# Performance work log

Measured on AMD Instinct MI355X. Metric: run time of the kernel, lower is better.

## Reference

```python
import jax, jax.numpy as jnp
import numpy as np

N_NODES = 50000


def gcn_conv(h, src, dst, W, b, n):
    # PyG GCNConv: x' = D^{-1/2} (A + I) D^{-1/2} (h W) + b
    x = h @ W  # [N, out]
    deg = jax.ops.segment_sum(jnp.ones_like(src, dtype=x.dtype), dst, num_segments=n) + 1.0  # self-loop
    dis = deg ** -0.5
    norm = dis[src] * dis[dst]  # [E]
    msg = x[src] * norm[:, None]  # [E, out]
    agg = jax.ops.segment_sum(msg, dst, num_segments=n)
    agg = agg + x * (dis * dis)[:, None]  # self-loop term: 1/deg_i * x_i
    return agg + b


def setup_inputs() -> dict:
    key = jax.random.key(0)
    ks = jax.random.split(key, 8)
    n, e = N_NODES, 800000
    d_in, d_rni, h = 128, 32, 256
    x = jax.random.normal(ks[0], (n, d_in), dtype=jnp.float32)
    rni = jax.random.normal(ks[1], (n, d_rni), dtype=jnp.float32)
    edge_index = jax.random.randint(ks[2], (2, e), 0, n, dtype=jnp.int64)
    s1 = (d_in + d_rni) ** -0.5
    s2 = h ** -0.5
    W1 = jax.random.normal(ks[3], (d_in + d_rni, h), dtype=jnp.float32) * s1
    b1 = jnp.zeros((h,), dtype=jnp.float32)
    W2 = jax.random.normal(ks[4], (h, h), dtype=jnp.float32) * s2
    b2 = jnp.zeros((h,), dtype=jnp.float32)
    W_out = jax.random.normal(ks[5], (h, h), dtype=jnp.float32) * s2
    b_out = jnp.zeros((h,), dtype=jnp.float32)
    return {"x": x, "rni": rni, "edge_index": edge_index, "W1": W1, "b1": b1,
            "W2": W2, "b2": b2, "W_out": W_out, "b_out": b_out}


def reference(x, rni, edge_index, W1, b1, W2, b2, W_out, b_out):
    n = x.shape[0]
    src, dst = edge_index[0], edge_index[1]
    h = jnp.concatenate([x, rni], axis=-1)  # RNI concat
    h = jax.nn.relu(gcn_conv(h, src, dst, W1, b1, n))
    h = jax.nn.relu(gcn_conv(h, src, dst, W2, b2, n))
    return h @ W_out + b_out
```

## Files before the change

### kernel.cpp

```cpp
#include <hip/hip_runtime.h>
#include <hip/hip_bf16.h>
#include <hip/hip_fp16.h>
#include <math.h>

#define D_IN   128
#define D_RNI  32
#define HID    256

typedef _Float16 half8 __attribute__((ext_vector_type(8)));
typedef float    f32x4 __attribute__((ext_vector_type(4)));

__global__ void k_detect(const unsigned int* __restrict__ w, int nwords, int* __restrict__ mode) {
    __shared__ unsigned int red[256];
    unsigned int acc = 0;
    for (int i = threadIdx.x; i < 1024; i += 256) {
        int idx = 2 * i + 1;
        if (idx < nwords) acc |= w[idx];
    }
    red[threadIdx.x] = acc;
    __syncthreads();
    for (int s = 128; s > 0; s >>= 1) {
        if (threadIdx.x < s) red[threadIdx.x] |= red[threadIdx.x + s];
        __syncthreads();
    }
    if (threadIdx.x == 0) *mode = (red[0] == 0u) ? 1 : 0;
}

__global__ void k_count(const unsigned int* __restrict__ ew, const int* __restrict__ mode_p,
                        int* __restrict__ counts, int e) {
    int mode = *mode_p;
    int i = blockIdx.x * 256 + threadIdx.x;
    if (i >= e) return;
    int d = mode ? (int)ew[2 * ((size_t)e + i)] : (int)ew[(size_t)e + i];
    atomicAdd(&counts[d], 1);
}

__global__ __launch_bounds__(1024) void k_scan1(const int* __restrict__ counts,
                                                int* __restrict__ incl,
                                                int* __restrict__ bsum, int n) {
    __shared__ int sd[1024];
    int t = threadIdx.x;
    int i = blockIdx.x * 1024 + t;
    int v = (i < n) ? counts[i] : 0;
    sd[t] = v;
    __syncthreads();
    for (int off = 1; off < 1024; off <<= 1) {
        int tmp = (t >= off) ? sd[t - off] : 0;
        __syncthreads();
        sd[t] += tmp;
        __syncthreads();
    }
    if (i < n) incl[i] = sd[t];
    if (t == 1023) bsum[blockIdx.x] = sd[1023];
}

__global__ __launch_bounds__(1024) void k_scan2(int* __restrict__ bsum, int nb) {
    __shared__ int sd[1024];
    int t = threadIdx.x;
    int v = (t < nb) ? bsum[t] : 0;
    sd[t] = v;
    __syncthreads();
    for (int off = 1; off < 1024; off <<= 1) {
        int tmp = (t >= off) ? sd[t - off] : 0;
        __syncthreads();
        sd[t] += tmp;
        __syncthreads();
    }
    if (t < nb) bsum[t] = sd[t] - v;
    if (t == nb - 1) bsum[nb] = sd[t];
}

__global__ void k_scan3(const int* __restrict__ counts, const int* __restrict__ incl,
                        const int* __restrict__ bsum,
                        int* __restrict__ rowptr, int* __restrict__ cursor,
                        float* __restrict__ dis, int n, int nb) {
    int i = blockIdx.x * 256 + threadIdx.x;
    if (i >= n) return;
    int excl = incl[i] - counts[i] + bsum[i >> 10];
    rowptr[i] = excl;
    cursor[i] = excl;
    dis[i] = 1.0f / sqrtf((float)(counts[i] + 1));
    if (i == 0) rowptr[n] = bsum[nb];
}

__global__ void k_scatter(const unsigned int* __restrict__ ew, const int* __restrict__ mode_p,
                          int* __restrict__ cursor, int* __restrict__ csr, int e) {
    int mode = *mode_p;
    int i = blockIdx.x * 256 + threadIdx.x;
    if (i >= e) return;
    int s, d;
    if (mode) {
        s = (int)ew[2 * (size_t)i];
        d = (int)ew[2 * ((size_t)e + i)];
    } else {
        s = (int)ew[(size_t)i];
        d = (int)ew[(size_t)e + i];
    }
    int pos = atomicAdd(&cursor[d], 1);
    csr[pos] = s;
}

__global__ void k_cvt_wt(const float* __restrict__ W, __half* __restrict__ Wt,
                         int K, int N, int total) {
    int i = blockIdx.x * 256 + threadIdx.x;
    if (i >= total) return;
    int k = i / N, nn = i - k * N;
    Wt[(size_t)nn * K + k] = __float2half(W[i]);
}

#define KT 32
#define LSTR 40
template <bool A_F32, bool ADD_BIAS, bool HALF_OUT>
__global__ __launch_bounds__(256) void k_mgemm(const void* __restrict__ Av, int strideA, int KA,
                                               const void* __restrict__ A2v, int strideA2,
                                               const __half* __restrict__ Bt,
                                               const float* __restrict__ bias,
                                               void* Cv, int M, int K) {
    __shared__ __half As[64 * LSTR];
    __shared__ __half Bs[256 * LSTR];
    int tid = threadIdx.x;
    int wave = tid >> 6, lane = tid & 63;
    int q = lane >> 4, m16 = lane & 15;
    int r0 = blockIdx.x * 64;

    f32x4 acc[4][4] = {};

    for (int k0 = 0; k0 < K; k0 += KT) {
        __syncthreads();
        {
            int r = tid >> 2, kq = (tid & 3) * 8;
            int row = r0 + r; if (row >= M) row = M - 1;
            if (A_F32) {
                const float* src; int stride, kk0;
                if (k0 < KA) { src = (const float*)Av;  stride = strideA;  kk0 = k0; }
                else         { src = (const float*)A2v; stride = strideA2; kk0 = k0 - KA; }
                const float* p = &src[(size_t)row * stride + kk0 + kq];
                float4 va = *reinterpret_cast<const float4*>(p);
                float4 vb = *reinterpret_cast<const float4*>(p + 4);
                union { __half2 h2[4]; uint4 u; } uu;
                uu.h2[0] = __floats2half2_rn(va.x, va.y);
                uu.h2[1] = __floats2half2_rn(va.z, va.w);
                uu.h2[2] = __floats2half2_rn(vb.x, vb.y);
                uu.h2[3] = __floats2half2_rn(vb.z, vb.w);
                *reinterpret_cast<uint4*>(&As[r * LSTR + kq]) = uu.u;
            } else {
                const __half* src = (const __half*)Av;
                uint4 v = *reinterpret_cast<const uint4*>(&src[(size_t)row * strideA + k0 + kq]);
                *reinterpret_cast<uint4*>(&As[r * LSTR + kq]) = v;
            }
        }
        {
            int nb = tid >> 2, kq = (tid & 3) * 8;
            #pragma unroll
            for (int i = 0; i < 4; ++i) {
                int nn = nb + i * 64;
                uint4 v = *reinterpret_cast<const uint4*>(&Bt[(size_t)nn * K + k0 + kq]);
                *reinterpret_cast<uint4*>(&Bs[nn * LSTR + kq]) = v;
            }
        }
        __syncthreads();

        half8 af[4], bf[4];
        #pragma unroll
        for (int mi = 0; mi < 4; ++mi)
            af[mi] = *reinterpret_cast<const half8*>(&As[(mi * 16 + m16) * LSTR + q * 8]);
        #pragma unroll
        for (int ni = 0; ni < 4; ++ni)
            bf[ni] = *reinterpret_cast<const half8*>(&Bs[(wave * 64 + ni * 16 + m16) * LSTR + q * 8]);
        #pragma unroll
        for (int mi = 0; mi < 4; ++mi)
            #pragma unroll
            for (int ni = 0; ni < 4; ++ni)
                acc[mi][ni] = __builtin_amdgcn_mfma_f32_16x16x32_f16(af[mi], bf[ni], acc[mi][ni], 0, 0, 0);
    }

    #pragma unroll
    for (int mi = 0; mi < 4; ++mi) {
        #pragma unroll
        for (int r = 0; r < 4; ++r) {
            int row = r0 + mi * 16 + q * 4 + r;
            if (row >= M) continue;
            #pragma unroll
            for (int ni = 0; ni < 4; ++ni) {
                int col = wave * 64 + ni * 16 + m16;
                float v = acc[mi][ni][r];
                if (ADD_BIAS) v += bias[col];
                if (HALF_OUT) ((__half*)Cv)[(size_t)row * HID + col] = __float2half(v);
                else          ((float*)Cv)[(size_t)row * HID + col] = v;
            }
        }
    }
}

__global__ __launch_bounds__(256) void k_agg(const __half* __restrict__ xh,
                                             const int* __restrict__ rowptr,
                                             const int* __restrict__ csr,
                                             const float* __restrict__ dis,
                                             const float* __restrict__ bias,
                                             __half* __restrict__ outh, int n) {
    int i = blockIdx.x * 4 + (threadIdx.x >> 6);
    if (i >= n) return;
    int lane = threadIdx.x & 63;
    int c4 = lane * 4;
    float disd = dis[i];
    int e0 = rowptr[i], e1 = rowptr[i + 1];

    float acc0, acc1, acc2, acc3;
    {
        uint2 v = *reinterpret_cast<const uint2*>(&xh[(size_t)i * HID + c4]);
        float2 f0 = __half22float2(*reinterpret_cast<__half2*>(&v.x));
        float2 f1 = __half22float2(*reinterpret_cast<__half2*>(&v.y));
        float ws = disd * disd;
        acc0 = f0.x * ws; acc1 = f0.y * ws; acc2 = f1.x * ws; acc3 = f1.y * ws;
    }

    for (int e = e0; e < e1; e += 64) {
        int cnt = min(64, e1 - e);
        int sreg = 0; float wreg = 0.0f;
        if (lane < cnt) {
            sreg = csr[e + lane];
            wreg = dis[sreg] * disd;
        }
        int j = 0;
        for (; j + 4 <= cnt; j += 4) {
            int   s0 = __shfl(sreg, j + 0), s1 = __shfl(sreg, j + 1);
            int   s2 = __shfl(sreg, j + 2), s3 = __shfl(sreg, j + 3);
            float w0 = __shfl(wreg, j + 0), w1 = __shfl(wreg, j + 1);
            float w2 = __shfl(wreg, j + 2), w3 = __shfl(wreg, j + 3);
            uint2 v0 = *reinterpret_cast<const uint2*>(&xh[(size_t)s0 * HID + c4]);
            uint2 v1 = *reinterpret_cast<const uint2*>(&xh[(size_t)s1 * HID + c4]);
            uint2 v2 = *reinterpret_cast<const uint2*>(&xh[(size_t)s2 * HID + c4]);
            uint2 v3 = *reinterpret_cast<const uint2*>(&xh[(size_t)s3 * HID + c4]);
            float2 a0 = __half22float2(*reinterpret_cast<__half2*>(&v0.x));
            float2 b0 = __half22float2(*reinterpret_cast<__half2*>(&v0.y));
            float2 a1 = __half22float2(*reinterpret_cast<__half2*>(&v1.x));
            float2 b1 = __half22float2(*reinterpret_cast<__half2*>(&v1.y));
            float2 a2 = __half22float2(*reinterpret_cast<__half2*>(&v2.x));
            float2 b2 = __half22float2(*reinterpret_cast<__half2*>(&v2.y));
            float2 a3 = __half22float2(*reinterpret_cast<__half2*>(&v3.x));
            float2 b3 = __half22float2(*reinterpret_cast<__half2*>(&v3.y));
            acc0 = fmaf(a0.x, w0, acc0); acc1 = fmaf(a0.y, w0, acc1);
            acc2 = fmaf(b0.x, w0, acc2); acc3 = fmaf(b0.y, w0, acc3);
            acc0 = fmaf(a1.x, w1, acc0); acc1 = fmaf(a1.y, w1, acc1);
            acc2 = fmaf(b1.x, w1, acc2); acc3 = fmaf(b1.y, w1, acc3);
            acc0 = fmaf(a2.x, w2, acc0); acc1 = fmaf(a2.y, w2, acc1);
            acc2 = fmaf(b2.x, w2, acc2); acc3 = fmaf(b2.y, w2, acc3);
            acc0 = fmaf(a3.x, w3, acc0); acc1 = fmaf(a3.y, w3, acc1);
            acc2 = fmaf(b3.x, w3, acc2); acc3 = fmaf(b3.y, w3, acc3);
        }
        for (; j < cnt; ++j) {
            int   s = __shfl(sreg, j);
            float w = __shfl(wreg, j);
            uint2 v = *reinterpret_cast<const uint2*>(&xh[(size_t)s * HID + c4]);
            float2 a = __half22float2(*reinterpret_cast<__half2*>(&v.x));
            float2 b = __half22float2(*reinterpret_cast<__half2*>(&v.y));
            acc0 = fmaf(a.x, w, acc0); acc1 = fmaf(a.y, w, acc1);
            acc2 = fmaf(b.x, w, acc2); acc3 = fmaf(b.y, w, acc3);
        }
    }

    float4 bb = *reinterpret_cast<const float4*>(&bias[c4]);
    union { __half2 h2[2]; uint2 u; } o;
    o.h2[0] = __floats2half2_rn(fmaxf(acc0 + bb.x, 0.0f), fmaxf(acc1 + bb.y, 0.0f));
    o.h2[1] = __floats2half2_rn(fmaxf(acc2 + bb.z, 0.0f), fmaxf(acc3 + bb.w, 0.0f));
    *reinterpret_cast<uint2*>(&outh[(size_t)i * HID + c4]) = o.u;
}

extern "C" void kernel_launch(void* const* d_in, const int* in_sizes, int n_in,
                              void* d_out, int out_size, void* d_ws, size_t ws_size,
                              hipStream_t stream) {
    const float* x     = (const float*)d_in[0];
    const float* rni   = (const float*)d_in[1];
    const unsigned int* ew = (const unsigned int*)d_in[2];
    const float* W1    = (const float*)d_in[3];
    const float* b1    = (const float*)d_in[4];
    const float* W2    = (const float*)d_in[5];
    const float* b2    = (const float*)d_in[6];
    const float* W_out = (const float*)d_in[7];
    const float* b_out = (const float*)d_in[8];
    float* out = (float*)d_out;

    const int n  = in_sizes[0] / D_IN;
    const int e  = in_sizes[2] / 2;
    const int nb = (n + 1023) / 1024;
    const int K1 = D_IN + D_RNI;

    char* ws = (char*)d_ws;
    size_t off = 0;
    auto carve = [&](size_t bytes) {
        char* p = ws + off;
        off = (off + bytes + 255) & ~(size_t)255;
        return p;
    };
    __half* xh    = (__half*)carve((size_t)n * HID * sizeof(__half));
    __half* h     = (__half*)carve((size_t)n * HID * sizeof(__half));
    __half* W1t   = (__half*)carve((size_t)K1 * HID * sizeof(__half));
    __half* W2t   = (__half*)carve((size_t)HID * HID * sizeof(__half));
    __half* Wot   = (__half*)carve((size_t)HID * HID * sizeof(__half));
    int*   counts = (int*)carve((size_t)n * sizeof(int));
    int*   incl   = (int*)carve((size_t)n * sizeof(int));
    int*   bsum   = (int*)carve((size_t)(nb + 1) * sizeof(int));
    int*   rowptr = (int*)carve((size_t)(n + 1) * sizeof(int));
    int*   cursor = (int*)carve((size_t)n * sizeof(int));
    float* dis    = (float*)carve((size_t)n * sizeof(float));
    int*   csr    = (int*)carve((size_t)e * sizeof(int));
    int*   mode   = (int*)carve(sizeof(int));
    (void)ws_size;

    const int eb = (e + 255) / 256;
    const int gemm_blocks = (n + 63) / 64;
    const int agg_blocks  = (n + 3) / 4;

    k_detect<<<1, 256, 0, stream>>>(ew, 2 * e, mode);
    hipMemsetAsync(counts, 0, (size_t)n * sizeof(int), stream);
    k_count<<<eb, 256, 0, stream>>>(ew, mode, counts, e);
    k_scan1<<<nb, 1024, 0, stream>>>(counts, incl, bsum, n);
    k_scan2<<<1, 1024, 0, stream>>>(bsum, nb);
    k_scan3<<<(n + 255) / 256, 256, 0, stream>>>(counts, incl, bsum, rowptr, cursor, dis, n, nb);
    k_scatter<<<eb, 256, 0, stream>>>(ew, mode, cursor, csr, e);

    {
        int tw1 = K1 * HID;
        k_cvt_wt<<<(tw1 + 255) / 256, 256, 0, stream>>>(W1, W1t, K1, HID, tw1);
        int tw = HID * HID;
        k_cvt_wt<<<(tw + 255) / 256, 256, 0, stream>>>(W2, W2t, HID, HID, tw);
        k_cvt_wt<<<(tw + 255) / 256, 256, 0, stream>>>(W_out, Wot, HID, HID, tw);
    }

    k_mgemm<true, false, true><<<gemm_blocks, 256, 0, stream>>>(x, D_IN, D_IN, rni, D_RNI,
                                                                W1t, nullptr, xh, n, K1);
    k_agg<<<agg_blocks, 256, 0, stream>>>(xh, rowptr, csr, dis, b1, h, n);

    k_mgemm<false, false, true><<<gemm_blocks, 256, 0, stream>>>(h, HID, HID, nullptr, 0,
                                                                 W2t, nullptr, xh, n, HID);
    k_agg<<<agg_blocks, 256, 0, stream>>>(xh, rowptr, csr, dis, b2, h, n);

    k_mgemm<false, true, false><<<gemm_blocks, 256, 0, stream>>>(h, HID, HID, nullptr, 0,
                                                                 Wot, b_out, out, n, HID);
}
```

Before: 386.1 us.

## Split aggregation columns across 8 blocks and process 8 edges per wave step

The aggregation kernel now launches 8 blocks per group of 4 nodes, each covering a 32-column slice of the 256-wide feature row. Within a wave, 8 lanes handle different edges at once while 8 lanes cover the slice, and the partial sums are combined with xor shuffles. This raises parallelism and memory-level concurrency for low-degree nodes, at the cost of reading csr/dis 8 times per node, extra shuffle reductions, and idle lanes when the edge count is not a multiple of 8. The csr load is also marked nontemporal.

Measured after the change: 607.3 us. +57.3%, slower.

```diff
diff --git a/kernel.cpp b/kernel.cpp
--- a/kernel.cpp
+++ b/kernel.cpp
@@ -198,72 +198,59 @@
                                              const float* __restrict__ dis,
                                              const float* __restrict__ bias,
                                              __half* __restrict__ outh, int n) {
-    int i = blockIdx.x * 4 + (threadIdx.x >> 6);
+    int g = blockIdx.x & 7;
+    int i = (blockIdx.x >> 3) * 4 + (threadIdx.x >> 6);
     if (i >= n) return;
     int lane = threadIdx.x & 63;
-    int c4 = lane * 4;
+    int esub = lane >> 3;
+    int cq   = lane & 7;
+    int cbase = g * 32 + cq * 4;
+    const __half* xcol = xh + cbase;
+
     float disd = dis[i];
     int e0 = rowptr[i], e1 = rowptr[i + 1];
 
-    float acc0, acc1, acc2, acc3;
-    {
-        uint2 v = *reinterpret_cast<const uint2*>(&xh[(size_t)i * HID + c4]);
-        float2 f0 = __half22float2(*reinterpret_cast<__half2*>(&v.x));
-        float2 f1 = __half22float2(*reinterpret_cast<__half2*>(&v.y));
-        float ws = disd * disd;
-        acc0 = f0.x * ws; acc1 = f0.y * ws; acc2 = f1.x * ws; acc3 = f1.y * ws;
-    }
+    float a0 = 0.0f, a1 = 0.0f, a2 = 0.0f, a3 = 0.0f;
 
     for (int e = e0; e < e1; e += 64) {
         int cnt = min(64, e1 - e);
         int sreg = 0; float wreg = 0.0f;
         if (lane < cnt) {
-            sreg = csr[e + lane];
+            sreg = __builtin_nontemporal_load(&csr[e + lane]);
             wreg = dis[sreg] * disd;
         }
-        int j = 0;
-        for (; j + 4 <= cnt; j += 4) {
-            int   s0 = __shfl(sreg, j + 0), s1 = __shfl(sreg, j + 1);
-            int   s2 = __shfl(sreg, j + 2), s3 = __shfl(sreg, j + 3);
-            float w0 = __shfl(wreg, j + 0), w1 = __shfl(wreg, j + 1);
-            float w2 = __shfl(wreg, j + 2), w3 = __shfl(wreg, j + 3);
-            uint2 v0 = *reinterpret_cast<const uint2*>(&xh[(size_t)s0 * HID + c4]);
-            uint2 v1 = *reinterpret_cast<const uint2*>(&xh[(size_t)s1 * HID + c4]);
-            uint2 v2 = *reinterpret_cast<const uint2*>(&xh[(size_t)s2 * HID + c4]);
-            uint2 v3 = *reinterpret_cast<const uint2*>(&xh[(size_t)s3 * HID + c4]);
-            float2 a0 = __half22float2(*reinterpret_cast<__half2*>(&v0.x));
-            float2 b0 = __half22float2(*reinterpret_cast<__half2*>(&v0.y));
-            float2 a1 = __half22float2(*reinterpret_cast<__half2*>(&v1.x));
-            float2 b1 = __half22float2(*reinterpret_cast<__half2*>(&v1.y));
-            float2 a2 = __half22float2(*reinterpret_cast<__half2*>(&v2.x));
-            float2 b2 = __half22float2(*reinterpret_cast<__half2*>(&v2.y));
-            float2 a3 = __half22float2(*reinterpret_cast<__half2*>(&v3.x));
-            float2 b3 = __half22float2(*reinterpret_cast<__half2*>(&v3.y));
-            acc0 = fmaf(a0.x, w0, acc0); acc1 = fmaf(a0.y, w0, acc1);
-            acc2 = fmaf(b0.x, w0, acc2); acc3 = fmaf(b0.y, w0, acc3);
-            acc0 = fmaf(a1.x, w1, acc0); acc1 = fmaf(a1.y, w1, acc1);
-            acc2 = fmaf(b1.x, w1, acc2); acc3 = fmaf(b1.y, w1, acc3);
-            acc0 = fmaf(a2.x, w2, acc0); acc1 = fmaf(a2.y, w2, acc1);
-            acc2 = fmaf(b2.x, w2, acc2); acc3 = fmaf(b2.y, w2, acc3);
-            acc0 = fmaf(a3.x, w3, acc0); acc1 = fmaf(a3.y, w3, acc1);
-            acc2 = fmaf(b3.x, w3, acc2); acc3 = fmaf(b3.y, w3, acc3);
-        }
-        for (; j < cnt; ++j) {
-            int   s = __shfl(sreg, j);
-            float w = __shfl(wreg, j);
-            uint2 v = *reinterpret_cast<const uint2*>(&xh[(size_t)s * HID + c4]);
-            float2 a = __half22float2(*reinterpret_cast<__half2*>(&v.x));
-            float2 b = __half22float2(*reinterpret_cast<__half2*>(&v.y));
-            acc0 = fmaf(a.x, w, acc0); acc1 = fmaf(a.y, w, acc1);
-            acc2 = fmaf(b.x, w, acc2); acc3 = fmaf(b.y, w, acc3);
-        }
-    }
-
-    float4 bb = *reinterpret_cast<const float4*>(&bias[c4]);
-    union { __half2 h2[2]; uint2 u; } o;
-    o.h2[0] = __floats2half2_rn(fmaxf(acc0 + bb.x, 0.0f), fmaxf(acc1 + bb.y, 0.0f));
-    o.h2[1] = __floats2half2_rn(fmaxf(acc2 + bb.z, 0.0f), fmaxf(acc3 + bb.w, 0.0f));
-    *reinterpret_cast<uint2*>(&outh[(size_t)i * HID + c4]) = o.u;
+        for (int j = 0; j < cnt; j += 8) {
+            int   s = __shfl(sreg, j + esub);
+            float w = __shfl(wreg, j + esub);
+            uint2 v = *reinterpret_cast<const uint2*>(&xcol[(size_t)s * HID]);
+            float2 f0 = __half22float2(*reinterpret_cast<__half2*>(&v.x));
+            float2 f1 = __half22float2(*reinterpret_cast<__half2*>(&v.y));
+            a0 = fmaf(f0.x, w, a0); a1 = fmaf(f0.y, w, a1);
+            a2 = fmaf(f1.x, w, a2); a3 = fmaf(f1.y, w, a3);
+        }
+    }
+
+    #pragma unroll
+    for (int m = 8; m < 64; m <<= 1) {
+        a0 += __shfl_xor(a0, m);
+        a1 += __shfl_xor(a1, m);
+        a2 += __shfl_xor(a2, m);
+        a3 += __shfl_xor(a3, m);
+    }
+
+    if (esub == 0) {
+        uint2 v = *reinterpret_cast<const uint2*>(&xcol[(size_t)i * HID]);
+        float2 f0 = __half22float2(*reinterpret_cast<__half2*>(&v.x));
+        float2 f1 = __half22float2(*reinterpret_cast<__half2*>(&v.y));
+        float ws = disd * disd;
+        a0 = fmaf(f0.x, ws, a0); a1 = fmaf(f0.y, ws, a1);
+        a2 = fmaf(f1.x, ws, a2); a3 = fmaf(f1.y, ws, a3);
+        float4 bb = *reinterpret_cast<const float4*>(&bias[cbase]);
+        union { __half2 h2[2]; uint2 u; } o;
+        o.h2[0] = __floats2half2_rn(fmaxf(a0 + bb.x, 0.0f), fmaxf(a1 + bb.y, 0.0f));
+        o.h2[1] = __floats2half2_rn(fmaxf(a2 + bb.z, 0.0f), fmaxf(a3 + bb.w, 0.0f));
+        *reinterpret_cast<uint2*>(&outh[(size_t)i * HID + cbase]) = o.u;
+    }
 }
 
 extern "C" void kernel_launch(void* const* d_in, const int* in_sizes, int n_in,
@@ -309,7 +296,7 @@
 
     const int eb = (e + 255) / 256;
     const int gemm_blocks = (n + 63) / 64;
-    const int agg_blocks  = (n + 3) / 4;
+    const int agg_blocks  = ((n + 3) / 4) * 8;
 
     k_detect<<<1, 256, 0, stream>>>(ew, 2 * e, mode);
     hipMemsetAsync(counts, 0, (size_t)n * sizeof(int), stream);
```

## Enlarge GEMM tile to 128 rows and prefetch next K-slice into registers

Applied to the files above, without the earlier changes.

The dense GEMM kernel now uses 512 threads arranged as a 2x4 wave grid over a 128x256 output tile, which halves how often the shared B-weight tile is reloaded per output row. It also prefetches the next K slice of A and B into registers while the current slice's MFMAs run, so global latency can overlap with compute. In exchange the kernel uses more registers and LDS per block and launches half as many blocks, which may lower occupancy.

After: 368.3 us. 4.6% less time.

```diff
diff --git a/kernel.cpp b/kernel.cpp
--- a/kernel.cpp
+++ b/kernel.cpp
@@ -111,62 +111,77 @@
 #define KT 32
 #define LSTR 40
 template <bool A_F32, bool ADD_BIAS, bool HALF_OUT>
-__global__ __launch_bounds__(256) void k_mgemm(const void* __restrict__ Av, int strideA, int KA,
+__global__ __launch_bounds__(512) void k_mgemm(const void* __restrict__ Av, int strideA, int KA,
                                                const void* __restrict__ A2v, int strideA2,
                                                const __half* __restrict__ Bt,
                                                const float* __restrict__ bias,
                                                void* Cv, int M, int K) {
-    __shared__ __half As[64 * LSTR];
+    __shared__ __half As[128 * LSTR];
     __shared__ __half Bs[256 * LSTR];
     int tid = threadIdx.x;
     int wave = tid >> 6, lane = tid & 63;
+    int wm = wave >> 2, wn = wave & 3;
     int q = lane >> 4, m16 = lane & 15;
-    int r0 = blockIdx.x * 64;
+    int r0 = blockIdx.x * 128;
+
+    int ar  = tid >> 2, akq = (tid & 3) * 8;
+    int br  = tid >> 1, bkq = (tid & 1) * 16;
+
+    int arow = r0 + ar; if (arow >= M) arow = M - 1;
 
     f32x4 acc[4][4] = {};
 
+    float4 afr0, afr1;
+    uint4  areg;
+    uint4  breg0, breg1;
+
+    auto loadA = [&](int k0) {
+        if (A_F32) {
+            const float* src; int stride, kk0;
+            if (k0 < KA) { src = (const float*)Av;  stride = strideA;  kk0 = k0; }
+            else         { src = (const float*)A2v; stride = strideA2; kk0 = k0 - KA; }
+            const float* p = &src[(size_t)arow * stride + kk0 + akq];
+            afr0 = *reinterpret_cast<const float4*>(p);
+            afr1 = *reinterpret_cast<const float4*>(p + 4);
+        } else {
+            const __half* src = (const __half*)Av;
+            areg = *reinterpret_cast<const uint4*>(&src[(size_t)arow * strideA + k0 + akq]);
+        }
+    };
+    auto loadB = [&](int k0) {
+        const __half* p = &Bt[(size_t)br * K + k0 + bkq];
+        breg0 = *reinterpret_cast<const uint4*>(p);
+        breg1 = *reinterpret_cast<const uint4*>(p + 8);
+    };
+    auto writeLDS = [&]() {
+        if (A_F32) {
+            union { __half2 h2[4]; uint4 u; } uu;
+            uu.h2[0] = __floats2half2_rn(afr0.x, afr0.y);
+            uu.h2[1] = __floats2half2_rn(afr0.z, afr0.w);
+            uu.h2[2] = __floats2half2_rn(afr1.x, afr1.y);
+            uu.h2[3] = __floats2half2_rn(afr1.z, afr1.w);
+            *reinterpret_cast<uint4*>(&As[ar * LSTR + akq]) = uu.u;
+        } else {
+            *reinterpret_cast<uint4*>(&As[ar * LSTR + akq]) = areg;
+        }
+        *reinterpret_cast<uint4*>(&Bs[br * LSTR + bkq])     = breg0;
+        *reinterpret_cast<uint4*>(&Bs[br * LSTR + bkq + 8]) = breg1;
+    };
+
+    loadA(0); loadB(0);
     for (int k0 = 0; k0 < K; k0 += KT) {
         __syncthreads();
-        {
-            int r = tid >> 2, kq = (tid & 3) * 8;
-            int row = r0 + r; if (row >= M) row = M - 1;
-            if (A_F32) {
-                const float* src; int stride, kk0;
-                if (k0 < KA) { src = (const float*)Av;  stride = strideA;  kk0 = k0; }
-                else         { src = (const float*)A2v; stride = strideA2; kk0 = k0 - KA; }
-                const float* p = &src[(size_t)row * stride + kk0 + kq];
-                float4 va = *reinterpret_cast<const float4*>(p);
-                float4 vb = *reinterpret_cast<const float4*>(p + 4);
-                union { __half2 h2[4]; uint4 u; } uu;
-                uu.h2[0] = __floats2half2_rn(va.x, va.y);
-                uu.h2[1] = __floats2half2_rn(va.z, va.w);
-                uu.h2[2] = __floats2half2_rn(vb.x, vb.y);
-                uu.h2[3] = __floats2half2_rn(vb.z, vb.w);
-                *reinterpret_cast<uint4*>(&As[r * LSTR + kq]) = uu.u;
-            } else {
-                const __half* src = (const __half*)Av;
-                uint4 v = *reinterpret_cast<const uint4*>(&src[(size_t)row * strideA + k0 + kq]);
-                *reinterpret_cast<uint4*>(&As[r * LSTR + kq]) = v;
-            }
-        }
-        {
-            int nb = tid >> 2, kq = (tid & 3) * 8;
-            #pragma unroll
-            for (int i = 0; i < 4; ++i) {
-                int nn = nb + i * 64;
-                uint4 v = *reinterpret_cast<const uint4*>(&Bt[(size_t)nn * K + k0 + kq]);
-                *reinterpret_cast<uint4*>(&Bs[nn * LSTR + kq]) = v;
-            }
-        }
-        __syncthreads();
+        writeLDS();
+        __syncthreads();
+        if (k0 + KT < K) { loadA(k0 + KT); loadB(k0 + KT); }
 
         half8 af[4], bf[4];
         #pragma unroll
         for (int mi = 0; mi < 4; ++mi)
-            af[mi] = *reinterpret_cast<const half8*>(&As[(mi * 16 + m16) * LSTR + q * 8]);
+            af[mi] = *reinterpret_cast<const half8*>(&As[(wm * 64 + mi * 16 + m16) * LSTR + q * 8]);
         #pragma unroll
         for (int ni = 0; ni < 4; ++ni)
-            bf[ni] = *reinterpret_cast<const half8*>(&Bs[(wave * 64 + ni * 16 + m16) * LSTR + q * 8]);
+            bf[ni] = *reinterpret_cast<const half8*>(&Bs[(wn * 64 + ni * 16 + m16) * LSTR + q * 8]);
         #pragma unroll
         for (int mi = 0; mi < 4; ++mi)
             #pragma unroll
@@ -178,11 +193,11 @@
     for (int mi = 0; mi < 4; ++mi) {
         #pragma unroll
         for (int r = 0; r < 4; ++r) {
-            int row = r0 + mi * 16 + q * 4 + r;
+            int row = r0 + wm * 64 + mi * 16 + q * 4 + r;
             if (row >= M) continue;
             #pragma unroll
             for (int ni = 0; ni < 4; ++ni) {
-                int col = wave * 64 + ni * 16 + m16;
+                int col = wn * 64 + ni * 16 + m16;
                 float v = acc[mi][ni][r];
                 if (ADD_BIAS) v += bias[col];
                 if (HALF_OUT) ((__half*)Cv)[(size_t)row * HID + col] = __float2half(v);
@@ -308,7 +323,7 @@
     (void)ws_size;
 
     const int eb = (e + 255) / 256;
-    const int gemm_blocks = (n + 63) / 64;
+    const int gemm_blocks = (n + 127) / 128;
     const int agg_blocks  = (n + 3) / 4;
 
     k_detect<<<1, 256, 0, stream>>>(ew, 2 * e, mode);
@@ -327,14 +342,14 @@
         k_cvt_wt<<<(tw + 255) / 256, 256, 0, stream>>>(W_out, Wot, HID, HID, tw);
     }
 
-    k_mgemm<true, false, true><<<gemm_blocks, 256, 0, stream>>>(x, D_IN, D_IN, rni, D_RNI,
+    k_mgemm<true, false, true><<<gemm_blocks, 512, 0, stream>>>(x, D_IN, D_IN, rni, D_RNI,
                                                                 W1t, nullptr, xh, n, K1);
     k_agg<<<agg_blocks, 256, 0, stream>>>(xh, rowptr, csr, dis, b1, h, n);
 
-    k_mgemm<false, false, true><<<gemm_blocks, 256, 0, stream>>>(h, HID, HID, nullptr, 0,
+    k_mgemm<false, false, true><<<gemm_blocks, 512, 0, stream>>>(h, HID, HID, nullptr, 0,
                                                                  W2t, nullptr, xh, n, HID);
     k_agg<<<agg_blocks, 256, 0, stream>>>(xh, rowptr, csr, dis, b2, h, n);
 
-    k_mgemm<false, true, false><<<gemm_blocks, 256, 0, stream>>>(h, HID, HID, nullptr, 0,
+    k_mgemm<false, true, false><<<gemm_blocks, 512, 0, stream>>>(h, HID, HID, nullptr, 0,
                                                                  Wot, b_out, out, n, HID);
 }
```
